# Performance work log

Measured on AMD Instinct MI355X. Metric: run time of the kernel, lower is better.

The kernel has to match this reference:

```python
import jax, jax.numpy as jnp
import numpy as np

N = 100_000      # nodes
E = 3_200_000    # directed edges
F_IN = 128       # node feature dim
H = 16           # hidden channels


def setup_inputs() -> dict:
    key = jax.random.key(0)
    k0, k1, k2, k3, k4, k5 = jax.random.split(key, 6)
    x = jax.random.normal(k0, (N, F_IN), dtype=jnp.float32)
    edge_index = jax.random.randint(k1, (2, E), 0, N, dtype=jnp.int32)
    W1 = jax.random.normal(k2, (F_IN, H), dtype=jnp.float32) * (1.0 / np.sqrt(F_IN))
    b1 = jax.random.normal(k3, (H,), dtype=jnp.float32) * 0.02
    W2 = jax.random.normal(k4, (H, 1), dtype=jnp.float32) * (1.0 / np.sqrt(H))
    b2 = jax.random.normal(k5, (1,), dtype=jnp.float32) * 0.02
    return {"x": x, "edge_index": edge_index, "W1": W1, "b1": b1, "W2": W2, "b2": b2}


def _gcn_conv(x, src, dst, deg_inv_sqrt, W, b):
    # PyG GCNConv: h = x @ W; out_i = sum_{j->i} norm_ij * h_j + b
    # norm_ij = deg_i^-1/2 * deg_j^-1/2 (degrees include self-loops)
    n = x.shape[0]
    h = x @ W                                   # [N, out]
    norm = deg_inv_sqrt[src] * deg_inv_sqrt[dst]  # [E+N]
    msg = h[src] * norm[:, None]                # gather + scale
    out = jax.ops.segment_sum(msg, dst, num_segments=n)
    return out + b


def reference(x, edge_index, W1, b1, W2, b2):
    n = x.shape[0]
    loops = jnp.arange(n, dtype=edge_index.dtype)
    src = jnp.concatenate([edge_index[0], loops])  # self-loops appended
    dst = jnp.concatenate([edge_index[1], loops])
    # degree of destination nodes (with self-loops), shared by both layers
    deg = jax.ops.segment_sum(jnp.ones_like(dst, dtype=x.dtype), dst, num_segments=n)
    deg_inv_sqrt = jax.lax.rsqrt(jnp.maximum(deg, 1.0))  # deg >= 1 due to self-loops

    h = jax.nn.relu(_gcn_conv(x, src, dst, deg_inv_sqrt, W1, b1))
    out = _gcn_conv(h, src, dst, deg_inv_sqrt, W2, b2)
    return out
```

## Files before the change

kernel.cpp:

```cpp
#include <hip/hip_runtime.h>
#include <hip/hip_fp16.h>

#define FIN 128
#define HC 16
#define NB 391
#define NSL 391
#define BKT 256
#define CELL 64
#define STRIDE 80
#define ESLICE 8188

typedef _Float16 half8 __attribute__((ext_vector_type(8)));
typedef float f32x4 __attribute__((ext_vector_type(4)));

__global__ __launch_bounds__(1024) void scatter_kernel(const int* __restrict__ src,
                                                       const int* __restrict__ dst,
                                                       unsigned int* __restrict__ ebuf,
                                                       unsigned char* __restrict__ cntcell, int E) {
    __shared__ int cur[NB];
    int blk = blockIdx.x, t = threadIdx.x;
    for (int i = t; i < NB; i += 1024) cur[i] = 0;
    __syncthreads();
    int s = blk * ESLICE, e = min(E, s + ESLICE);
    int boff = blk * CELL;
    if (s < e) {
        int n4 = (e - s) >> 2;
        const int4* d4 = (const int4*)(dst + s);
        const int4* s4 = (const int4*)(src + s);
        for (int i = t; i < n4; i += 1024) {
            int4 dd = d4[i];
            int4 ss = s4[i];
            int b0 = dd.x >> 8, p0 = atomicAdd(&cur[b0], 1);
            ebuf[(size_t)b0 * (NSL * CELL) + boff + p0] = ((unsigned)ss.x << 8) | (unsigned)(dd.x & 255);
            int b1 = dd.y >> 8, p1 = atomicAdd(&cur[b1], 1);
            ebuf[(size_t)b1 * (NSL * CELL) + boff + p1] = ((unsigned)ss.y << 8) | (unsigned)(dd.y & 255);
            int b2 = dd.z >> 8, p2 = atomicAdd(&cur[b2], 1);
            ebuf[(size_t)b2 * (NSL * CELL) + boff + p2] = ((unsigned)ss.z << 8) | (unsigned)(dd.z & 255);
            int b3 = dd.w >> 8, p3 = atomicAdd(&cur[b3], 1);
            ebuf[(size_t)b3 * (NSL * CELL) + boff + p3] = ((unsigned)ss.w << 8) | (unsigned)(dd.w & 255);
        }
    }
    __syncthreads();
    for (int i = t; i < NB; i += 1024) cntcell[(size_t)blk * NB + i] = (unsigned char)cur[i];
}

__global__ __launch_bounds__(1024) void sortdis_kernel(const unsigned int* __restrict__ ebuf,
                                                       const unsigned char* __restrict__ cntcell,
                                                       int* __restrict__ csr, int* __restrict__ deg,
                                                       float* __restrict__ dis, int n) {
    __shared__ int cnt[BKT];
    __shared__ unsigned char cc[NB];
    int b = blockIdx.x, t = threadIdx.x;
    if (t < BKT) cnt[t] = 0;
    for (int i = t; i < NB; i += 1024) cc[i] = cntcell[(size_t)i * NB + b];
    __syncthreads();
    int wave = t >> 6, lane = t & 63;
    size_t cbase = (size_t)b * BKT * STRIDE;
    size_t ebase = (size_t)b * (NSL * CELL);
    for (int c = wave; c < NSL; c += 16) {
        int m = cc[c];
        if (lane < m) {
            unsigned u = ebuf[ebase + (size_t)c * CELL + lane];
            int l = u & 255;
            int r = atomicAdd(&cnt[l], 1);
            csr[cbase + l * STRIDE + r] = (int)(u >> 8);
        }
    }
    __syncthreads();
    if (t < BKT) {
        int node = b * BKT + t;
        if (node < n) {
            deg[node] = cnt[t];
            dis[node] = rsqrtf((float)cnt[t] + 1.0f);
        }
    }
}

__global__ void h1_mfma_kernel(const float* __restrict__ x, const float* __restrict__ W1,
                               const float* __restrict__ dis, __half* __restrict__ hs16, int n) {
    __shared__ float xs[64][132];
    int t = threadIdx.x;
    int wave = t >> 6;
    int lane = t & 63;
    int r = lane & 15, g = lane >> 4;
    int rowbase0 = blockIdx.x * 64;
#pragma unroll
    for (int it = 0; it < 8; ++it) {
        int i = it * 256 + t;
        int row = i >> 5, c4 = i & 31;
        int grow = rowbase0 + row;
        const float4* xr = (const float4*)(x + (size_t)(grow < n ? grow : n - 1) * FIN);
        float4 v = xr[c4];
        xs[row][c4 * 4 + 0] = v.x;
        xs[row][c4 * 4 + 1] = v.y;
        xs[row][c4 * 4 + 2] = v.z;
        xs[row][c4 * 4 + 3] = v.w;
    }
    half8 bfrag[4];
#pragma unroll
    for (int i = 0; i < 4; ++i)
#pragma unroll
        for (int j = 0; j < 8; ++j)
            bfrag[i][j] = (_Float16)W1[(i * 32 + g * 8 + j) * HC + r];
    __syncthreads();
    int rowbase = wave * 16;
    f32x4 acc = {0.f, 0.f, 0.f, 0.f};
#pragma unroll
    for (int i = 0; i < 4; ++i) {
        const float4* rowp = (const float4*)&xs[rowbase + r][i * 32 + g * 8];
        float4 v0 = rowp[0];
        float4 v1 = rowp[1];
        half8 afrag;
        afrag[0] = (_Float16)v0.x; afrag[1] = (_Float16)v0.y;
        afrag[2] = (_Float16)v0.z; afrag[3] = (_Float16)v0.w;
        afrag[4] = (_Float16)v1.x; afrag[5] = (_Float16)v1.y;
        afrag[6] = (_Float16)v1.z; afrag[7] = (_Float16)v1.w;
        acc = __builtin_amdgcn_mfma_f32_16x16x32_f16(afrag, bfrag[i], acc, 0, 0, 0);
    }
#pragma unroll
    for (int j = 0; j < 4; ++j) {
        int orow = rowbase0 + rowbase + g * 4 + j;
        if (orow < n) hs16[(size_t)orow * HC + r] = __float2half(acc[j] * dis[orow]);
    }
}

#define GSTEP2(T, SIDX, MM, AX, AY)                                         \
    {                                                                       \
        int e_ = (T) * 8 + eg;                                              \
        int s_ = __shfl((SIDX), e_);                                        \
        float2 f_ = __half22float2(hs16[(size_t)s_ * 8 + cp]);              \
        if (e_ < (MM)) { (AX) += f_.x; (AY) += f_.y; }                      \
    }

__global__ void pull_layer1_kernel(const int* __restrict__ deg, const int* __restrict__ csr,
                                   const __half2* __restrict__ hs16,
                                   const float* __restrict__ b1, const float* __restrict__ W2,
                                   float* __restrict__ h2s, int n) {
    int wid = (blockIdx.x * blockDim.x + threadIdx.x) >> 6;
    int n0 = wid * 2;
    if (n0 >= n) return;
    int n1 = n0 + 1;
    int lane = threadIdx.x & 63;
    int cp = lane & 7;
    int eg = lane >> 3;
    int p0 = csr[n0 * STRIDE + lane];
    int p1 = csr[n1 * STRIDE + lane];
    int2 mpair = ((const int2*)deg)[wid];
    int m0 = mpair.x, m1 = mpair.y;
    int c0 = (lane < m0) ? p0 : 0;
    int c1 = (lane < m1) ? p1 : 0;
    int mm0 = min(m0, 64), mm1 = min(m1, 64);
    float ax0 = 0.f, ay0 = 0.f, ax1 = 0.f, ay1 = 0.f;
    GSTEP2(0, c0, mm0, ax0, ay0) GSTEP2(0, c1, mm1, ax1, ay1)
    GSTEP2(1, c0, mm0, ax0, ay0) GSTEP2(1, c1, mm1, ax1, ay1)
    GSTEP2(2, c0, mm0, ax0, ay0) GSTEP2(2, c1, mm1, ax1, ay1)
    GSTEP2(3, c0, mm0, ax0, ay0) GSTEP2(3, c1, mm1, ax1, ay1)
    if (mm0 > 32) {
        GSTEP2(4, c0, mm0, ax0, ay0) GSTEP2(5, c0, mm0, ax0, ay0)
        GSTEP2(6, c0, mm0, ax0, ay0) GSTEP2(7, c0, mm0, ax0, ay0)
        for (int k = 64 + eg; k < m0; k += 8) {
            float2 f = __half22float2(hs16[(size_t)csr[n0 * STRIDE + k] * 8 + cp]);
            ax0 += f.x; ay0 += f.y;
        }
    }
    if (mm1 > 32) {
        GSTEP2(4, c1, mm1, ax1, ay1) GSTEP2(5, c1, mm1, ax1, ay1)
        GSTEP2(6, c1, mm1, ax1, ay1) GSTEP2(7, c1, mm1, ax1, ay1)
        for (int k = 64 + eg; k < m1; k += 8) {
            float2 f = __half22float2(hs16[(size_t)csr[n1 * STRIDE + k] * 8 + cp]);
            ax1 += f.x; ay1 += f.y;
        }
    }
    ax0 += __shfl_xor(ax0, 8);  ay0 += __shfl_xor(ay0, 8);
    ax1 += __shfl_xor(ax1, 8);  ay1 += __shfl_xor(ay1, 8);
    ax0 += __shfl_xor(ax0, 16); ay0 += __shfl_xor(ay0, 16);
    ax1 += __shfl_xor(ax1, 16); ay1 += __shfl_xor(ay1, 16);
    ax0 += __shfl_xor(ax0, 32); ay0 += __shfl_xor(ay0, 32);
    ax1 += __shfl_xor(ax1, 32); ay1 += __shfl_xor(ay1, 32);
    float2 self0 = __half22float2(hs16[(size_t)n0 * 8 + cp]);
    float2 self1 = __half22float2(hs16[(size_t)n1 * 8 + cp]);
    float bb = b1[2 * cp], bb2 = b1[2 * cp + 1];
    float w = W2[2 * cp], w2 = W2[2 * cp + 1];
    float d0 = rsqrtf((float)m0 + 1.0f);
    float d1 = rsqrtf((float)m1 + 1.0f);
    float v0 = fmaxf(fmaf(d0, ax0 + self0.x, bb), 0.f) * w
             + fmaxf(fmaf(d0, ay0 + self0.y, bb2), 0.f) * w2;
    float v1 = fmaxf(fmaf(d1, ax1 + self1.x, bb), 0.f) * w
             + fmaxf(fmaf(d1, ay1 + self1.y, bb2), 0.f) * w2;
    v0 += __shfl_xor(v0, 1); v1 += __shfl_xor(v1, 1);
    v0 += __shfl_xor(v0, 2); v1 += __shfl_xor(v1, 2);
    v0 += __shfl_xor(v0, 4); v1 += __shfl_xor(v1, 4);
    if (lane == 0) {
        h2s[n0] = v0 * d0;
        h2s[n1] = v1 * d1;
    }
}

__global__ void pull_layer2_kernel(const int* __restrict__ deg, const int* __restrict__ csr,
                                   const float* __restrict__ h2s,
                                   const float* __restrict__ b2, float* __restrict__ out, int n) {
    int g = blockIdx.x * blockDim.x + threadIdx.x;
    int node = g >> 4;
    if (node >= n) return;
    int q = g & 15;
    int start = node * STRIDE;
    int m = deg[node];
    float a = 0.f;
    int k = q;
    for (; k + 16 < m; k += 32) {
        int i0 = csr[start + k];
        int i1 = csr[start + k + 16];
        a += h2s[i0] + h2s[i1];
    }
    for (; k < m; k += 16) a += h2s[csr[start + k]];
    a += __shfl_xor(a, 1);
    a += __shfl_xor(a, 2);
    a += __shfl_xor(a, 4);
    a += __shfl_xor(a, 8);
    if (q == 0) out[node] = rsqrtf((float)m + 1.0f) * (a + h2s[node]) + b2[0];
}

extern "C" void kernel_launch(void* const* d_in, const int* in_sizes, int n_in,
                              void* d_out, int out_size, void* d_ws, size_t ws_size,
                              hipStream_t stream) {
    const float* x  = (const float*)d_in[0];
    const int* ei   = (const int*)d_in[1];
    const float* W1 = (const float*)d_in[2];
    const float* b1 = (const float*)d_in[3];
    const float* W2 = (const float*)d_in[4];
    const float* b2 = (const float*)d_in[5];
    float* out = (float*)d_out;

    const int n = in_sizes[0] / FIN;
    const int E = in_sizes[1] / 2;
    const int* src = ei;
    const int* dst = ei + E;

    const size_t EB = (size_t)NB * NSL * CELL;
    unsigned int* ebuf  = (unsigned int*)d_ws;
    int* csr            = (int*)(ebuf + EB);
    unsigned char* cc   = (unsigned char*)(csr + (size_t)100000 * STRIDE + 128);
    int* deg            = (int*)(cc + 152888);
    float* dis          = (float*)(deg + n);
    float* h2s          = dis + n;
    __half* hs16        = (__half*)(h2s + n);

    scatter_kernel<<<NSL, 1024, 0, stream>>>(src, dst, ebuf, cc, E);
    sortdis_kernel<<<NB, 1024, 0, stream>>>(ebuf, cc, csr, deg, dis, n);
    h1_mfma_kernel<<<(n + 63) / 64, 256, 0, stream>>>(x, W1, dis, hs16, n);
    pull_layer1_kernel<<<(n / 2 * 64 + 511) / 512, 512, 0, stream>>>(deg, csr, (const __half2*)hs16, b1, W2, h2s, n);
    pull_layer2_kernel<<<(n * 16 + 511) / 512, 512, 0, stream>>>(deg, csr, h2s, b2, out, n);
}
```

Measured before the change: 104.2 us.

## Fuse feature transform into sort kernel and widen layer-1 gather to 4 halves

The separate h1 MFMA kernel is folded into the bucket-sort kernel. Each 1024-thread block (16 waves) computes x@W1 for its own 256 nodes, reading x directly into registers rather than staging it through shared memory, and scales by a degree factor kept in shared memory. This removes one launch and one global round trip for dis. The layer-1 pull now has each lane load 4 halves (8 bytes) per edge, with 16 edges in flight per wave step instead of 8, which raises memory-level parallelism per gather. In exchange there are more shuffle reductions, and the sort kernel has higher register pressure.

```diff
diff --git a/kernel.cpp b/kernel.cpp
--- a/kernel.cpp
+++ b/kernel.cpp
@@ -44,12 +44,14 @@
     for (int i = t; i < NB; i += 1024) cntcell[(size_t)blk * NB + i] = (unsigned char)cur[i];
 }
 
-__global__ __launch_bounds__(1024) void sortdis_kernel(const unsigned int* __restrict__ ebuf,
-                                                       const unsigned char* __restrict__ cntcell,
-                                                       int* __restrict__ csr, int* __restrict__ deg,
-                                                       float* __restrict__ dis, int n) {
+__global__ __launch_bounds__(1024) void sortdis_h1_kernel(
+    const unsigned int* __restrict__ ebuf, const unsigned char* __restrict__ cntcell,
+    const float* __restrict__ x, const float* __restrict__ W1,
+    int* __restrict__ csr, int* __restrict__ deg, float* __restrict__ dis,
+    __half* __restrict__ hs16, int n) {
     __shared__ int cnt[BKT];
     __shared__ unsigned char cc[NB];
+    __shared__ float disL[BKT];
     int b = blockIdx.x, t = threadIdx.x;
     if (t < BKT) cnt[t] = 0;
     for (int i = t; i < NB; i += 1024) cc[i] = cntcell[(size_t)i * NB + b];
@@ -69,71 +71,64 @@
     __syncthreads();
     if (t < BKT) {
         int node = b * BKT + t;
+        float dv = rsqrtf((float)cnt[t] + 1.0f);
+        disL[t] = dv;
         if (node < n) {
             deg[node] = cnt[t];
-            dis[node] = rsqrtf((float)cnt[t] + 1.0f);
-        }
-    }
-}
-
-__global__ void h1_mfma_kernel(const float* __restrict__ x, const float* __restrict__ W1,
-                               const float* __restrict__ dis, __half* __restrict__ hs16, int n) {
-    __shared__ float xs[64][132];
-    int t = threadIdx.x;
-    int wave = t >> 6;
-    int lane = t & 63;
+            dis[node] = dv;
+        }
+    }
+    __syncthreads();
     int r = lane & 15, g = lane >> 4;
-    int rowbase0 = blockIdx.x * 64;
-#pragma unroll
-    for (int it = 0; it < 8; ++it) {
-        int i = it * 256 + t;
-        int row = i >> 5, c4 = i & 31;
-        int grow = rowbase0 + row;
-        const float4* xr = (const float4*)(x + (size_t)(grow < n ? grow : n - 1) * FIN);
-        float4 v = xr[c4];
-        xs[row][c4 * 4 + 0] = v.x;
-        xs[row][c4 * 4 + 1] = v.y;
-        xs[row][c4 * 4 + 2] = v.z;
-        xs[row][c4 * 4 + 3] = v.w;
-    }
     half8 bfrag[4];
 #pragma unroll
     for (int i = 0; i < 4; ++i)
 #pragma unroll
         for (int j = 0; j < 8; ++j)
             bfrag[i][j] = (_Float16)W1[(i * 32 + g * 8 + j) * HC + r];
-    __syncthreads();
-    int rowbase = wave * 16;
+    int lrow = wave * 16;
+    int grow = b * BKT + lrow + r;
+    const f32x4* xr = (const f32x4*)(x + (size_t)(grow < n ? grow : n - 1) * FIN);
+    f32x4 v[8];
+#pragma unroll
+    for (int i = 0; i < 4; ++i) {
+        int idx = i * 8 + g * 2;
+        v[2 * i] = xr[idx];
+        v[2 * i + 1] = xr[idx + 1];
+    }
     f32x4 acc = {0.f, 0.f, 0.f, 0.f};
 #pragma unroll
     for (int i = 0; i < 4; ++i) {
-        const float4* rowp = (const float4*)&xs[rowbase + r][i * 32 + g * 8];
-        float4 v0 = rowp[0];
-        float4 v1 = rowp[1];
         half8 afrag;
-        afrag[0] = (_Float16)v0.x; afrag[1] = (_Float16)v0.y;
-        afrag[2] = (_Float16)v0.z; afrag[3] = (_Float16)v0.w;
-        afrag[4] = (_Float16)v1.x; afrag[5] = (_Float16)v1.y;
-        afrag[6] = (_Float16)v1.z; afrag[7] = (_Float16)v1.w;
+        afrag[0] = (_Float16)v[2 * i][0]; afrag[1] = (_Float16)v[2 * i][1];
+        afrag[2] = (_Float16)v[2 * i][2]; afrag[3] = (_Float16)v[2 * i][3];
+        afrag[4] = (_Float16)v[2 * i + 1][0]; afrag[5] = (_Float16)v[2 * i + 1][1];
+        afrag[6] = (_Float16)v[2 * i + 1][2]; afrag[7] = (_Float16)v[2 * i + 1][3];
         acc = __builtin_amdgcn_mfma_f32_16x16x32_f16(afrag, bfrag[i], acc, 0, 0, 0);
     }
 #pragma unroll
     for (int j = 0; j < 4; ++j) {
-        int orow = rowbase0 + rowbase + g * 4 + j;
-        if (orow < n) hs16[(size_t)orow * HC + r] = __float2half(acc[j] * dis[orow]);
-    }
-}
-
-#define GSTEP2(T, SIDX, MM, AX, AY)                                         \
+        int lr = lrow + g * 4 + j;
+        int orow = b * BKT + lr;
+        if (orow < n) hs16[(size_t)orow * HC + r] = __float2half(acc[j] * disL[lr]);
+    }
+}
+
+#define GSTEP4(T, SIDX, MM, A01, A23)                                       \
     {                                                                       \
-        int e_ = (T) * 8 + eg;                                              \
+        int e_ = (T) * 16 + eg;                                             \
         int s_ = __shfl((SIDX), e_);                                        \
-        float2 f_ = __half22float2(hs16[(size_t)s_ * 8 + cp]);              \
-        if (e_ < (MM)) { (AX) += f_.x; (AY) += f_.y; }                      \
+        uint2 raw_ = *(const uint2*)(hs16 + (size_t)s_ * 16 + cp4 * 4);     \
+        float2 f01_ = __half22float2(*(__half2*)&raw_.x);                   \
+        float2 f23_ = __half22float2(*(__half2*)&raw_.y);                   \
+        if (e_ < (MM)) {                                                    \
+            (A01).x += f01_.x; (A01).y += f01_.y;                           \
+            (A23).x += f23_.x; (A23).y += f23_.y;                           \
+        }                                                                   \
     }
 
 __global__ void pull_layer1_kernel(const int* __restrict__ deg, const int* __restrict__ csr,
-                                   const __half2* __restrict__ hs16,
+                                   const __half* __restrict__ hs16,
                                    const float* __restrict__ b1, const float* __restrict__ W2,
                                    float* __restrict__ h2s, int n) {
     int wid = (blockIdx.x * blockDim.x + threadIdx.x) >> 6;
@@ -141,8 +136,8 @@
     if (n0 >= n) return;
     int n1 = n0 + 1;
     int lane = threadIdx.x & 63;
-    int cp = lane & 7;
-    int eg = lane >> 3;
+    int cp4 = lane & 3;
+    int eg = lane >> 2;
     int p0 = csr[n0 * STRIDE + lane];
     int p1 = csr[n1 * STRIDE + lane];
     int2 mpair = ((const int2*)deg)[wid];
@@ -150,46 +145,57 @@
     int c0 = (lane < m0) ? p0 : 0;
     int c1 = (lane < m1) ? p1 : 0;
     int mm0 = min(m0, 64), mm1 = min(m1, 64);
-    float ax0 = 0.f, ay0 = 0.f, ax1 = 0.f, ay1 = 0.f;
-    GSTEP2(0, c0, mm0, ax0, ay0) GSTEP2(0, c1, mm1, ax1, ay1)
-    GSTEP2(1, c0, mm0, ax0, ay0) GSTEP2(1, c1, mm1, ax1, ay1)
-    GSTEP2(2, c0, mm0, ax0, ay0) GSTEP2(2, c1, mm1, ax1, ay1)
-    GSTEP2(3, c0, mm0, ax0, ay0) GSTEP2(3, c1, mm1, ax1, ay1)
+    float2 a010 = {0.f, 0.f}, a230 = {0.f, 0.f};
+    float2 a011 = {0.f, 0.f}, a231 = {0.f, 0.f};
+    GSTEP4(0, c0, mm0, a010, a230) GSTEP4(0, c1, mm1, a011, a231)
+    GSTEP4(1, c0, mm0, a010, a230) GSTEP4(1, c1, mm1, a011, a231)
     if (mm0 > 32) {
-        GSTEP2(4, c0, mm0, ax0, ay0) GSTEP2(5, c0, mm0, ax0, ay0)
-        GSTEP2(6, c0, mm0, ax0, ay0) GSTEP2(7, c0, mm0, ax0, ay0)
-        for (int k = 64 + eg; k < m0; k += 8) {
-            float2 f = __half22float2(hs16[(size_t)csr[n0 * STRIDE + k] * 8 + cp]);
-            ax0 += f.x; ay0 += f.y;
+        GSTEP4(2, c0, mm0, a010, a230) GSTEP4(3, c0, mm0, a010, a230)
+        for (int k = 64 + eg; k < m0; k += 16) {
+            int s_ = csr[n0 * STRIDE + k];
+            uint2 raw_ = *(const uint2*)(hs16 + (size_t)s_ * 16 + cp4 * 4);
+            float2 f01_ = __half22float2(*(__half2*)&raw_.x);
+            float2 f23_ = __half22float2(*(__half2*)&raw_.y);
+            a010.x += f01_.x; a010.y += f01_.y; a230.x += f23_.x; a230.y += f23_.y;
         }
     }
     if (mm1 > 32) {
-        GSTEP2(4, c1, mm1, ax1, ay1) GSTEP2(5, c1, mm1, ax1, ay1)
-        GSTEP2(6, c1, mm1, ax1, ay1) GSTEP2(7, c1, mm1, ax1, ay1)
-        for (int k = 64 + eg; k < m1; k += 8) {
-            float2 f = __half22float2(hs16[(size_t)csr[n1 * STRIDE + k] * 8 + cp]);
-            ax1 += f.x; ay1 += f.y;
-        }
-    }
-    ax0 += __shfl_xor(ax0, 8);  ay0 += __shfl_xor(ay0, 8);
-    ax1 += __shfl_xor(ax1, 8);  ay1 += __shfl_xor(ay1, 8);
-    ax0 += __shfl_xor(ax0, 16); ay0 += __shfl_xor(ay0, 16);
-    ax1 += __shfl_xor(ax1, 16); ay1 += __shfl_xor(ay1, 16);
-    ax0 += __shfl_xor(ax0, 32); ay0 += __shfl_xor(ay0, 32);
-    ax1 += __shfl_xor(ax1, 32); ay1 += __shfl_xor(ay1, 32);
-    float2 self0 = __half22float2(hs16[(size_t)n0 * 8 + cp]);
-    float2 self1 = __half22float2(hs16[(size_t)n1 * 8 + cp]);
-    float bb = b1[2 * cp], bb2 = b1[2 * cp + 1];
-    float w = W2[2 * cp], w2 = W2[2 * cp + 1];
+        GSTEP4(2, c1, mm1, a011, a231) GSTEP4(3, c1, mm1, a011, a231)
+        for (int k = 64 + eg; k < m1; k += 16) {
+            int s_ = csr[n1 * STRIDE + k];
+            uint2 raw_ = *(const uint2*)(hs16 + (size_t)s_ * 16 + cp4 * 4);
+            float2 f01_ = __half22float2(*(__half2*)&raw_.x);
+            float2 f23_ = __half22float2(*(__half2*)&raw_.y);
+            a011.x += f01_.x; a011.y += f01_.y; a231.x += f23_.x; a231.y += f23_.y;
+        }
+    }
+#pragma unroll
+    for (int off = 4; off < 64; off <<= 1) {
+        a010.x += __shfl_xor(a010.x, off); a010.y += __shfl_xor(a010.y, off);
+        a230.x += __shfl_xor(a230.x, off); a230.y += __shfl_xor(a230.y, off);
+        a011.x += __shfl_xor(a011.x, off); a011.y += __shfl_xor(a011.y, off);
+        a231.x += __shfl_xor(a231.x, off); a231.y += __shfl_xor(a231.y, off);
+    }
+    float4 bv = ((const float4*)b1)[cp4];
+    float4 wv = ((const float4*)W2)[cp4];
+    uint2 sr0 = *(const uint2*)(hs16 + (size_t)n0 * 16 + cp4 * 4);
+    uint2 sr1 = *(const uint2*)(hs16 + (size_t)n1 * 16 + cp4 * 4);
+    float2 s001 = __half22float2(*(__half2*)&sr0.x);
+    float2 s023 = __half22float2(*(__half2*)&sr0.y);
+    float2 s101 = __half22float2(*(__half2*)&sr1.x);
+    float2 s123 = __half22float2(*(__half2*)&sr1.y);
     float d0 = rsqrtf((float)m0 + 1.0f);
     float d1 = rsqrtf((float)m1 + 1.0f);
-    float v0 = fmaxf(fmaf(d0, ax0 + self0.x, bb), 0.f) * w
-             + fmaxf(fmaf(d0, ay0 + self0.y, bb2), 0.f) * w2;
-    float v1 = fmaxf(fmaf(d1, ax1 + self1.x, bb), 0.f) * w
-             + fmaxf(fmaf(d1, ay1 + self1.y, bb2), 0.f) * w2;
+    float v0 = fmaxf(fmaf(d0, a010.x + s001.x, bv.x), 0.f) * wv.x
+             + fmaxf(fmaf(d0, a010.y + s001.y, bv.y), 0.f) * wv.y
+             + fmaxf(fmaf(d0, a230.x + s023.x, bv.z), 0.f) * wv.z
+             + fmaxf(fmaf(d0, a230.y + s023.y, bv.w), 0.f) * wv.w;
+    float v1 = fmaxf(fmaf(d1, a011.x + s101.x, bv.x), 0.f) * wv.x
+             + fmaxf(fmaf(d1, a011.y + s101.y, bv.y), 0.f) * wv.y
+             + fmaxf(fmaf(d1, a231.x + s123.x, bv.z), 0.f) * wv.z
+             + fmaxf(fmaf(d1, a231.y + s123.y, bv.w), 0.f) * wv.w;
     v0 += __shfl_xor(v0, 1); v1 += __shfl_xor(v1, 1);
     v0 += __shfl_xor(v0, 2); v1 += __shfl_xor(v1, 2);
-    v0 += __shfl_xor(v0, 4); v1 += __shfl_xor(v1, 4);
     if (lane == 0) {
         h2s[n0] = v0 * d0;
         h2s[n1] = v1 * d1;
@@ -246,8 +252,7 @@
     __half* hs16        = (__half*)(h2s + n);
 
     scatter_kernel<<<NSL, 1024, 0, stream>>>(src, dst, ebuf, cc, E);
-    sortdis_kernel<<<NB, 1024, 0, stream>>>(ebuf, cc, csr, deg, dis, n);
-    h1_mfma_kernel<<<(n + 63) / 64, 256, 0, stream>>>(x, W1, dis, hs16, n);
-    pull_layer1_kernel<<<(n / 2 * 64 + 511) / 512, 512, 0, stream>>>(deg, csr, (const __half2*)hs16, b1, W2, h2s, n);
+    sortdis_h1_kernel<<<NB, 1024, 0, stream>>>(ebuf, cc, x, W1, csr, deg, dis, hs16, n);
+    pull_layer1_kernel<<<(n / 2 * 64 + 511) / 512, 512, 0, stream>>>(deg, csr, hs16, b1, W2, h2s, n);
     pull_layer2_kernel<<<(n * 16 + 511) / 512, 512, 0, stream>>>(deg, csr, h2s, b2, out, n);
 }
```

New measurement: 107.6 us. +3.3%, slower.
